# Kernel optimization log

Measured on AMD Instinct MI355X. Metric: run time of the kernel, lower is better.

Reference implementation:

```python
import jax, jax.numpy as jnp
import numpy as np

NUM_ENVS = 16384
N = 12          # decision vars (4 legs x 3D force)
M_CON = 24      # 4 SOC cones (3 each) + 12-dim hardtanh box
A_MIN, A_MAX = -10.0, 10.0
ALPHA, BETA = 1.0, 1.0


def setup_inputs() -> dict:
    key = jax.random.key(0)
    k1, k2, k3, k4 = jax.random.split(key, 4)
    Mw = jax.random.normal(k1, (NUM_ENVS, N, N), dtype=jnp.float32) / np.sqrt(N)
    # P must be SPD for inv/solve as in the original QP setup
    P = Mw @ jnp.swapaxes(Mw, -1, -2) + jnp.eye(N, dtype=jnp.float32)
    q = jax.random.normal(k2, (NUM_ENVS, N), dtype=jnp.float32)
    H = jax.random.normal(k3, (NUM_ENVS, M_CON, N), dtype=jnp.float32) * 0.5
    b = jax.random.normal(k4, (NUM_ENVS, M_CON), dtype=jnp.float32)
    contact_filter = jnp.ones((NUM_ENVS, M_CON), dtype=jnp.float32)
    return {"P": P, "q": q, "H": H, "b": b, "contact_filter": contact_filter, "iters": 100}


def _project(z, cf):
    # z: [B, m, 1]. Faithful to torch: project_onto_soc's only in-place effect on z
    # is z_part *= (z_part[:, 2:3] > 0); the full cone projection result is
    # discarded (returned but never written back). Then hardtanh box, then contact filter.
    Bsz = z.shape[0]
    soc = z[:, :12].reshape(Bsz, 4, 3)               # 4 cones of dim 3
    soc = soc * (soc[:, :, 2:3] > 0)                 # zero cone block if z-component <= 0
    box = jnp.clip(z[:, 12:24], A_MIN, A_MAX)        # hardtanh
    z = jnp.concatenate([soc.reshape(Bsz, 12, 1), box], axis=1)
    return z * cf


def reference(P, q, H, b, contact_filter, iters):
    m = H.shape[1]
    q_ = q[..., None]                                # [B, n, 1]
    b_ = b[..., None]                                # [B, m, 1]
    cf = contact_filter[..., None]                   # [B, m, 1]
    Ht = jnp.swapaxes(H, -1, -2)
    I = jnp.eye(m, dtype=P.dtype)
    Fm = I - H @ jnp.linalg.inv(P + Ht @ H) @ Ht     # [B, m, m]
    mu = Fm @ (H @ jnp.linalg.solve(P, q_) - b_)     # [B, m, 1]
    A = jnp.concatenate([
        jnp.concatenate([Fm, BETA * Fm], axis=2),
        jnp.concatenate([ALPHA * (I - 2.0 * Fm), I - 2.0 * ALPHA * BETA * Fm], axis=2),
    ], axis=1)                                       # [B, 2m, 2m]
    Bv = jnp.concatenate([BETA * mu, -2.0 * ALPHA * BETA * mu], axis=1)  # [B, 2m, 1]

    def step(lz, _):
        lz = A @ lz + Bv
        lz = jnp.concatenate([lz[:, :m], _project(lz[:, m:], cf)], axis=1)
        return lz, None

    lz0 = jnp.zeros((P.shape[0], 2 * m, 1), dtype=P.dtype)
    lz, _ = jax.lax.scan(step, lz0, None, length=iters)
    x = jnp.linalg.pinv(H) @ (lz[:, m:] - b_)        # [B, n, 1]
    return x, lz
```

## Files before the change

kernel.cpp:

```cpp
#include <hip/hip_runtime.h>

#define EPB 8
#define BLOCK 64
#define HS 292
#define GS 148
#define SS 28

#define WFENCE() __builtin_amdgcn_wave_barrier()

#define FMA4(acc, f, s)                                         \
  acc = fmaf((f).x, (s).x,                                      \
        fmaf((f).y, (s).y,                                      \
        fmaf((f).z, (s).z,                                      \
        fmaf((f).w, (s).w, (acc)))))

#define VFMA(acc, s, v)                                         \
  { (acc).x = fmaf((s), (v).x, (acc).x);                        \
    (acc).y = fmaf((s), (v).y, (acc).y);                        \
    (acc).z = fmaf((s), (v).z, (acc).z);                        \
    (acc).w = fmaf((s), (v).w, (acc).w); }

struct Row6 { float4 c0, c1, c2, c3, c4, c5; };

template<int K>
__device__ __forceinline__ float getel(const float4& a, const float4& b, const float4& c) {
  if constexpr (K == 0) return a.x; else if constexpr (K == 1) return a.y;
  else if constexpr (K == 2) return a.z; else if constexpr (K == 3) return a.w;
  else if constexpr (K == 4) return b.x; else if constexpr (K == 5) return b.y;
  else if constexpr (K == 6) return b.z; else if constexpr (K == 7) return b.w;
  else if constexpr (K == 8) return c.x; else if constexpr (K == 9) return c.y;
  else if constexpr (K == 10) return c.z; else return c.w;
}
template<int K>
__device__ __forceinline__ void setel(float4& a, float4& b, float4& c, float v) {
  if constexpr (K == 0) a.x = v; else if constexpr (K == 1) a.y = v;
  else if constexpr (K == 2) a.z = v; else if constexpr (K == 3) a.w = v;
  else if constexpr (K == 4) b.x = v; else if constexpr (K == 5) b.y = v;
  else if constexpr (K == 6) b.z = v; else if constexpr (K == 7) b.w = v;
  else if constexpr (K == 8) c.x = v; else if constexpr (K == 9) c.y = v;
  else if constexpr (K == 10) c.z = v; else c.w = v;
}

template<int K>
__device__ __forceinline__ void gj_step(float* A, int t) {
  if (t == K || t + 8 == K) {
    float4* r = (float4*)(A + K * 12);
    float4 a = r[0], b = r[1], c = r[2];
    float ip = 1.0f / getel<K>(a, b, c);
    setel<K>(a, b, c, 1.0f);
    a.x *= ip; a.y *= ip; a.z *= ip; a.w *= ip;
    b.x *= ip; b.y *= ip; b.z *= ip; b.w *= ip;
    c.x *= ip; c.y *= ip; c.z *= ip; c.w *= ip;
    r[0] = a; r[1] = b; r[2] = c;
  }
  WFENCE();
  const float4* pr = (const float4*)(A + K * 12);
  float4 p0 = pr[0], p1 = pr[1], p2 = pr[2];
  {
    float4* rr = (float4*)(A + t * 12);
    float4 a = rr[0], b = rr[1], c = rr[2];
    float f = getel<K>(a, b, c);
    if (t == K) f = 0.0f; else setel<K>(a, b, c, 0.0f);
    a.x = fmaf(-f, p0.x, a.x); a.y = fmaf(-f, p0.y, a.y);
    a.z = fmaf(-f, p0.z, a.z); a.w = fmaf(-f, p0.w, a.w);
    b.x = fmaf(-f, p1.x, b.x); b.y = fmaf(-f, p1.y, b.y);
    b.z = fmaf(-f, p1.z, b.z); b.w = fmaf(-f, p1.w, b.w);
    c.x = fmaf(-f, p2.x, c.x); c.y = fmaf(-f, p2.y, c.y);
    c.z = fmaf(-f, p2.z, c.z); c.w = fmaf(-f, p2.w, c.w);
    rr[0] = a; rr[1] = b; rr[2] = c;
  }
  if (t < 4) {
    const int i = t + 8;
    float4* rr = (float4*)(A + i * 12);
    float4 a = rr[0], b = rr[1], c = rr[2];
    float f = getel<K>(a, b, c);
    if (i == K) f = 0.0f; else setel<K>(a, b, c, 0.0f);
    a.x = fmaf(-f, p0.x, a.x); a.y = fmaf(-f, p0.y, a.y);
    a.z = fmaf(-f, p0.z, a.z); a.w = fmaf(-f, p0.w, a.w);
    b.x = fmaf(-f, p1.x, b.x); b.y = fmaf(-f, p1.y, b.y);
    b.z = fmaf(-f, p1.z, b.z); b.w = fmaf(-f, p1.w, b.w);
    c.x = fmaf(-f, p2.x, c.x); c.y = fmaf(-f, p2.y, c.y);
    c.z = fmaf(-f, p2.z, c.z); c.w = fmaf(-f, p2.w, c.w);
    rr[0] = a; rr[1] = b; rr[2] = c;
  }
  WFENCE();
}
template<int K>
__device__ __forceinline__ void gj_all(float* A, int t) {
  gj_step<K>(A, t);
  if constexpr (K < 11) gj_all<K + 1>(A, t);
}

__device__ __forceinline__ float dot12(float4 a0, float4 a1, float4 a2,
                                       const float* p) {
  const float4* p4 = (const float4*)p;
  float4 b0 = p4[0], b1 = p4[1], b2 = p4[2];
  float acc = 0.f;
  FMA4(acc, a0, b0); FMA4(acc, a1, b1); FMA4(acc, a2, b2);
  return acc;
}

__device__ __forceinline__ void build_gram_row(const float* myH, float* gi,
                                               int i, bool addP) {
  float4 a0 = {0,0,0,0}, a1 = {0,0,0,0}, a2 = {0,0,0,0};
#pragma unroll
  for (int k = 0; k < 24; ++k) {
    float coef = myH[k * 12 + i];
    const float4* hk = (const float4*)(myH + k * 12);
    float4 h0 = hk[0], h1 = hk[1], h2 = hk[2];
    VFMA(a0, coef, h0); VFMA(a1, coef, h1); VFMA(a2, coef, h2);
  }
  float4* g = (float4*)(gi + i * 12);
  if (addP) {
    float4 q0 = g[0], q1 = g[1], q2 = g[2];
    a0.x += q0.x; a0.y += q0.y; a0.z += q0.z; a0.w += q0.w;
    a1.x += q1.x; a1.y += q1.y; a1.z += q1.z; a1.w += q1.w;
    a2.x += q2.x; a2.y += q2.y; a2.z += q2.z; a2.w += q2.w;
  }
  g[0] = a0; g[1] = a1; g[2] = a2;
}

__device__ __forceinline__ Row6 build_row(const float* myH, const float* gi, int r) {
  const float4* hr4 = (const float4*)(myH + r * 12);
  float4 h0 = hr4[0], h1 = hr4[1], h2 = hr4[2];
  float4 gA = {0,0,0,0}, gB = {0,0,0,0}, gC = {0,0,0,0};
#define ACC_G(c, coef)                                          \
  { const float4* g4 = (const float4*)(gi + (c) * 12);          \
    float4 r0 = g4[0], r1 = g4[1], r2 = g4[2];                  \
    VFMA(gA, coef, r0); VFMA(gB, coef, r1); VFMA(gC, coef, r2); }
  ACC_G(0, h0.x) ACC_G(1, h0.y) ACC_G(2,  h0.z) ACC_G(3,  h0.w)
  ACC_G(4, h1.x) ACC_G(5, h1.y) ACC_G(6,  h1.z) ACC_G(7,  h1.w)
  ACC_G(8, h2.x) ACC_G(9, h2.y) ACC_G(10, h2.z) ACC_G(11, h2.w)
#undef ACC_G
  Row6 R;
#define FEL(j) ((((j) == r) ? 1.0f : 0.0f) - dot12(gA, gB, gC, myH + (j) * 12))
  R.c0 = make_float4(FEL(0),  FEL(1),  FEL(2),  FEL(3));
  R.c1 = make_float4(FEL(4),  FEL(5),  FEL(6),  FEL(7));
  R.c2 = make_float4(FEL(8),  FEL(9),  FEL(10), FEL(11));
  R.c3 = make_float4(FEL(12), FEL(13), FEL(14), FEL(15));
  R.c4 = make_float4(FEL(16), FEL(17), FEL(18), FEL(19));
  R.c5 = make_float4(FEL(20), FEL(21), FEL(22), FEL(23));
#undef FEL
  return R;
}

__global__ __launch_bounds__(BLOCK)
void pdhg_kernel(const float* __restrict__ P, const float* __restrict__ q,
                 const float* __restrict__ H, const float* __restrict__ b,
                 const float* __restrict__ cf, const int* __restrict__ itp,
                 float* __restrict__ out, int Btot) {
  __shared__ __align__(16) float sH[EPB * HS];
  __shared__ __align__(16) float sGi[EPB * GS];
  __shared__ __align__(16) float sS[EPB * SS];
  __shared__ __align__(16) float sAux[EPB * SS];

  const int tid = threadIdx.x;
  const int e   = tid >> 3;
  const int t   = tid & 7;
  const int env = blockIdx.x * EPB + e;
  const int niter = itp[0];
  const int r0w = 3 * t;

  {
    const float4* gH = (const float4*)(H + (size_t)blockIdx.x * EPB * 288);
#pragma unroll
    for (int rep = 0; rep < 9; ++rep) {
      int i = tid + rep * 64;
      int ee = i / 72, off = i - ee * 72;
      *(float4*)&sH[ee * HS + off * 4] = gH[i];
    }
    const float4* gP = (const float4*)(P + (size_t)blockIdx.x * EPB * 144);
#pragma unroll
    for (int rep = 0; rep < 4; ++rep) {
      int i = tid + rep * 64;
      int ee = i / 36, off = i - ee * 36;
      *(float4*)&sGi[ee * GS + off * 4] = gP[i];
    }
    { int i = tid + 256; if (tid < 32) {
        int ee = i / 36, off = i - ee * 36;
        *(float4*)&sGi[ee * GS + off * 4] = gP[i]; } }
    const float4* gq = (const float4*)(q + (size_t)blockIdx.x * EPB * 12);
    if (tid < EPB * 3) {
      int ee = tid / 3, off = tid - ee * 3;
      *(float4*)&sAux[ee * SS + off * 4] = gq[tid];
    }
    const float4* gb = (const float4*)(b + (size_t)blockIdx.x * EPB * 24);
    if (tid < EPB * 6) {
      int ee = tid / 6, off = tid - ee * 6;
      *(float4*)&sS[ee * SS + off * 4] = gb[tid];
    }
  }
  WFENCE();

  const float* myH = &sH[e * HS];
  float* giB = &sGi[e * GS];
  float* auxB = &sAux[e * SS];
  const float* bB = &sS[e * SS];

  build_gram_row(myH, giB, t, true);
  if (t < 4) build_gram_row(myH, giB, t + 8, true);
  WFENCE();
  gj_all<0>(giB, t);

  {
    const float4* gr = (const float4*)(giB + t * 12);
    auxB[12 + t] = dot12(gr[0], gr[1], gr[2], auxB);
    if (t < 4) {
      const float4* gr8 = (const float4*)(giB + (t + 8) * 12);
      auxB[12 + t + 8] = dot12(gr8[0], gr8[1], gr8[2], auxB);
    }
  }
  WFENCE();

  Row6 F0 = build_row(myH, giB, r0w + 0);
  Row6 F1 = build_row(myH, giB, r0w + 1);
  Row6 F2 = build_row(myH, giB, r0w + 2);
  float mu0, mu1, mu2;
  {
    const float4* h0 = (const float4*)(myH + (r0w + 0) * 12);
    const float4* h1 = (const float4*)(myH + (r0w + 1) * 12);
    const float4* h2 = (const float4*)(myH + (r0w + 2) * 12);
    const float* y = auxB + 12;
    float u0 = dot12(h0[0], h0[1], h0[2], y);
    float u1 = dot12(h1[0], h1[1], h1[2], y);
    float u2 = dot12(h2[0], h2[1], h2[2], y);
    const float4* bv = (const float4*)bB;
    float d0 = 0.f, d1 = 0.f, d2 = 0.f;
    float4 v;
    v = bv[0]; FMA4(d0, F0.c0, v); FMA4(d1, F1.c0, v); FMA4(d2, F2.c0, v);
    v = bv[1]; FMA4(d0, F0.c1, v); FMA4(d1, F1.c1, v); FMA4(d2, F2.c1, v);
    v = bv[2]; FMA4(d0, F0.c2, v); FMA4(d1, F1.c2, v); FMA4(d2, F2.c2, v);
    v = bv[3]; FMA4(d0, F0.c3, v); FMA4(d1, F1.c3, v); FMA4(d2, F2.c3, v);
    v = bv[4]; FMA4(d0, F0.c4, v); FMA4(d1, F1.c4, v); FMA4(d2, F2.c4, v);
    v = bv[5]; FMA4(d0, F0.c5, v); FMA4(d1, F1.c5, v); FMA4(d2, F2.c5, v);
    mu0 = u0 - d0;
    mu1 = u1 - d1;
    mu2 = u2 - d2;
  }
  float cfr0 = cf[(size_t)env * 24 + r0w];
  float cfr1 = cf[(size_t)env * 24 + r0w + 1];
  float cfr2 = cf[(size_t)env * 24 + r0w + 2];

  float l0 = 0.f, l1 = 0.f, l2 = 0.f, z0 = 0.f, z1 = 0.f, z2 = 0.f;
  float* sw = &sS[e * SS];
  for (int it = 0; it < niter; ++it) {
    float s0 = l0 + z0, s1 = l1 + z1, s2 = l2 + z2;
    sw[r0w] = s0; sw[r0w + 1] = s1; sw[r0w + 2] = s2;
    WFENCE();
    const float4* sv = (const float4*)sw;
    float w0 = mu0, w1 = mu1, w2 = mu2;
    float4 c;
    c = sv[0]; FMA4(w0, F0.c0, c); FMA4(w1, F1.c0, c); FMA4(w2, F2.c0, c);
    c = sv[1]; FMA4(w0, F0.c1, c); FMA4(w1, F1.c1, c); FMA4(w2, F2.c1, c);
    c = sv[2]; FMA4(w0, F0.c2, c); FMA4(w1, F1.c2, c); FMA4(w2, F2.c2, c);
    c = sv[3]; FMA4(w0, F0.c3, c); FMA4(w1, F1.c3, c); FMA4(w2, F2.c3, c);
    c = sv[4]; FMA4(w0, F0.c4, c); FMA4(w1, F1.c4, c); FMA4(w2, F2.c4, c);
    c = sv[5]; FMA4(w0, F0.c5, c); FMA4(w1, F1.c5, c); FMA4(w2, F2.c5, c);
    WFENCE();
    float zp0 = fmaf(-2.0f, w0, s0);
    float zp1 = fmaf(-2.0f, w1, s1);
    float zp2 = fmaf(-2.0f, w2, s2);
    l0 = w0; l1 = w1; l2 = w2;
    if (t < 4) {
      float m = (zp2 > 0.0f) ? 1.0f : 0.0f;
      z0 = zp0 * m * cfr0; z1 = zp1 * m * cfr1; z2 = zp2 * m * cfr2;
    } else {
      z0 = fminf(fmaxf(zp0, -10.0f), 10.0f) * cfr0;
      z1 = fminf(fmaxf(zp1, -10.0f), 10.0f) * cfr1;
      z2 = fminf(fmaxf(zp2, -10.0f), 10.0f) * cfr2;
    }
  }

  float* xout  = out;
  float* lzout = out + (size_t)Btot * 12;
  lzout[(size_t)env * 48 + r0w]          = l0;
  lzout[(size_t)env * 48 + r0w + 1]      = l1;
  lzout[(size_t)env * 48 + r0w + 2]      = l2;
  lzout[(size_t)env * 48 + 24 + r0w]     = z0;
  lzout[(size_t)env * 48 + 24 + r0w + 1] = z1;
  lzout[(size_t)env * 48 + 24 + r0w + 2] = z2;

  float bo0 = b[(size_t)env * 24 + r0w];
  float bo1 = b[(size_t)env * 24 + r0w + 1];
  float bo2 = b[(size_t)env * 24 + r0w + 2];
  WFENCE();
  auxB[r0w]     = z0 - bo0;
  auxB[r0w + 1] = z1 - bo1;
  auxB[r0w + 2] = z2 - bo2;
  WFENCE();

  float rv0 = 0.f, rv8 = 0.f;
#pragma unroll
  for (int k = 0; k < 24; ++k) rv0 = fmaf(myH[k * 12 + t], auxB[k], rv0);
  if (t < 4) {
#pragma unroll
    for (int k = 0; k < 24; ++k) rv8 = fmaf(myH[k * 12 + t + 8], auxB[k], rv8);
  }
  build_gram_row(myH, giB, t, false);
  if (t < 4) build_gram_row(myH, giB, t + 8, false);
  WFENCE();
  auxB[t] = rv0;
  if (t < 4) auxB[t + 8] = rv8;
  WFENCE();

  gj_all<0>(giB, t);
  {
    const float4* gr = (const float4*)(giB + t * 12);
    xout[(size_t)env * 12 + t] = dot12(gr[0], gr[1], gr[2], auxB);
    if (t < 4) {
      const float4* gr8 = (const float4*)(giB + (t + 8) * 12);
      xout[(size_t)env * 12 + t + 8] = dot12(gr8[0], gr8[1], gr8[2], auxB);
    }
  }
}

extern "C" void kernel_launch(void* const* d_in, const int* in_sizes, int n_in,
                              void* d_out, int out_size, void* d_ws, size_t ws_size,
                              hipStream_t stream) {
  const float* P  = (const float*)d_in[0];
  const float* q  = (const float*)d_in[1];
  const float* H  = (const float*)d_in[2];
  const float* b  = (const float*)d_in[3];
  const float* cf = (const float*)d_in[4];
  const int*   it = (const int*)d_in[5];
  float* out = (float*)d_out;
  const int B = in_sizes[1] / 12;
  const int grid = B / EPB;
  pdhg_kernel<<<grid, BLOCK, 0, stream>>>(P, q, H, b, cf, it, out, B);
}
```

Measured before the change: 156.7 us.

## Replace LDS vector exchange with DPP butterfly reduction in PDHG iteration

Each iteration used to write its three lane values of s to shared memory and read back all 24 before doing the row-times-vector products. The new loop relies on the symmetry of Fm. Each lane forms partial products for all 24 outputs from its own three s values, sums them across the 8 lanes of an environment with three DPP steps (xor1, xor2, half-mirror), then selects its three outputs with a tree of lane-bit conditionals. This removes the LDS round trip and the wave barriers from the serial iteration chain, at the cost of about 72 extra DPP adds per iteration and more register pressure.

```diff
diff --git a/kernel.cpp b/kernel.cpp
--- a/kernel.cpp
+++ b/kernel.cpp
@@ -8,6 +8,10 @@
 
 #define WFENCE() __builtin_amdgcn_wave_barrier()
 
+#define DPP_XOR1 0xB1
+#define DPP_XOR2 0x4E
+#define DPP_HMIR 0x141
+
 #define FMA4(acc, f, s)                                         \
   acc = fmaf((f).x, (s).x,                                      \
         fmaf((f).y, (s).y,                                      \
@@ -20,7 +24,22 @@
     (acc).z = fmaf((s), (v).z, (acc).z);                        \
     (acc).w = fmaf((s), (v).w, (acc).w); }
 
-struct Row6 { float4 c0, c1, c2, c3, c4, c5; };
+struct Row6  { float4 a, b, c, d, e, f; };
+struct Vec24 { float4 a, b, c, d, e, f; };
+
+template<int CTRL>
+__device__ __forceinline__ float dppv(float v) {
+  return __int_as_float(__builtin_amdgcn_update_dpp(
+      0, __float_as_int(v), CTRL, 0xF, 0xF, true));
+}
+
+#define APPLY24(OP)                                              \
+  OP(a, x) OP(a, y) OP(a, z) OP(a, w)                            \
+  OP(b, x) OP(b, y) OP(b, z) OP(b, w)                            \
+  OP(c, x) OP(c, y) OP(c, z) OP(c, w)                            \
+  OP(d, x) OP(d, y) OP(d, z) OP(d, w)                            \
+  OP(e, x) OP(e, y) OP(e, z) OP(e, w)                            \
+  OP(f, x) OP(f, y) OP(f, z) OP(f, w)
 
 template<int K>
 __device__ __forceinline__ float getel(const float4& a, const float4& b, const float4& c) {
@@ -134,12 +153,12 @@
 #undef ACC_G
   Row6 R;
 #define FEL(j) ((((j) == r) ? 1.0f : 0.0f) - dot12(gA, gB, gC, myH + (j) * 12))
-  R.c0 = make_float4(FEL(0),  FEL(1),  FEL(2),  FEL(3));
-  R.c1 = make_float4(FEL(4),  FEL(5),  FEL(6),  FEL(7));
-  R.c2 = make_float4(FEL(8),  FEL(9),  FEL(10), FEL(11));
-  R.c3 = make_float4(FEL(12), FEL(13), FEL(14), FEL(15));
-  R.c4 = make_float4(FEL(16), FEL(17), FEL(18), FEL(19));
-  R.c5 = make_float4(FEL(20), FEL(21), FEL(22), FEL(23));
+  R.a = make_float4(FEL(0),  FEL(1),  FEL(2),  FEL(3));
+  R.b = make_float4(FEL(4),  FEL(5),  FEL(6),  FEL(7));
+  R.c = make_float4(FEL(8),  FEL(9),  FEL(10), FEL(11));
+  R.d = make_float4(FEL(12), FEL(13), FEL(14), FEL(15));
+  R.e = make_float4(FEL(16), FEL(17), FEL(18), FEL(19));
+  R.f = make_float4(FEL(20), FEL(21), FEL(22), FEL(23));
 #undef FEL
   return R;
 }
@@ -151,7 +170,7 @@
                  float* __restrict__ out, int Btot) {
   __shared__ __align__(16) float sH[EPB * HS];
   __shared__ __align__(16) float sGi[EPB * GS];
-  __shared__ __align__(16) float sS[EPB * SS];
+  __shared__ __align__(16) float sB[EPB * SS];
   __shared__ __align__(16) float sAux[EPB * SS];
 
   const int tid = threadIdx.x;
@@ -187,7 +206,7 @@
     const float4* gb = (const float4*)(b + (size_t)blockIdx.x * EPB * 24);
     if (tid < EPB * 6) {
       int ee = tid / 6, off = tid - ee * 6;
-      *(float4*)&sS[ee * SS + off * 4] = gb[tid];
+      *(float4*)&sB[ee * SS + off * 4] = gb[tid];
     }
   }
   WFENCE();
@@ -195,7 +214,7 @@
   const float* myH = &sH[e * HS];
   float* giB = &sGi[e * GS];
   float* auxB = &sAux[e * SS];
-  const float* bB = &sS[e * SS];
+  const float* bB = &sB[e * SS];
 
   build_gram_row(myH, giB, t, true);
   if (t < 4) build_gram_row(myH, giB, t + 8, true);
@@ -212,9 +231,9 @@
   }
   WFENCE();
 
-  Row6 F0 = build_row(myH, giB, r0w + 0);
-  Row6 F1 = build_row(myH, giB, r0w + 1);
-  Row6 F2 = build_row(myH, giB, r0w + 2);
+  Row6 Fc0 = build_row(myH, giB, r0w + 0);
+  Row6 Fc1 = build_row(myH, giB, r0w + 1);
+  Row6 Fc2 = build_row(myH, giB, r0w + 2);
   float mu0, mu1, mu2;
   {
     const float4* h0 = (const float4*)(myH + (r0w + 0) * 12);
@@ -227,12 +246,12 @@
     const float4* bv = (const float4*)bB;
     float d0 = 0.f, d1 = 0.f, d2 = 0.f;
     float4 v;
-    v = bv[0]; FMA4(d0, F0.c0, v); FMA4(d1, F1.c0, v); FMA4(d2, F2.c0, v);
-    v = bv[1]; FMA4(d0, F0.c1, v); FMA4(d1, F1.c1, v); FMA4(d2, F2.c1, v);
-    v = bv[2]; FMA4(d0, F0.c2, v); FMA4(d1, F1.c2, v); FMA4(d2, F2.c2, v);
-    v = bv[3]; FMA4(d0, F0.c3, v); FMA4(d1, F1.c3, v); FMA4(d2, F2.c3, v);
-    v = bv[4]; FMA4(d0, F0.c4, v); FMA4(d1, F1.c4, v); FMA4(d2, F2.c4, v);
-    v = bv[5]; FMA4(d0, F0.c5, v); FMA4(d1, F1.c5, v); FMA4(d2, F2.c5, v);
+    v = bv[0]; FMA4(d0, Fc0.a, v); FMA4(d1, Fc1.a, v); FMA4(d2, Fc2.a, v);
+    v = bv[1]; FMA4(d0, Fc0.b, v); FMA4(d1, Fc1.b, v); FMA4(d2, Fc2.b, v);
+    v = bv[2]; FMA4(d0, Fc0.c, v); FMA4(d1, Fc1.c, v); FMA4(d2, Fc2.c, v);
+    v = bv[3]; FMA4(d0, Fc0.d, v); FMA4(d1, Fc1.d, v); FMA4(d2, Fc2.d, v);
+    v = bv[4]; FMA4(d0, Fc0.e, v); FMA4(d1, Fc1.e, v); FMA4(d2, Fc2.e, v);
+    v = bv[5]; FMA4(d0, Fc0.f, v); FMA4(d1, Fc1.f, v); FMA4(d2, Fc2.f, v);
     mu0 = u0 - d0;
     mu1 = u1 - d1;
     mu2 = u2 - d2;
@@ -241,22 +260,42 @@
   float cfr1 = cf[(size_t)env * 24 + r0w + 1];
   float cfr2 = cf[(size_t)env * 24 + r0w + 2];
 
+  const bool tb0 = (t & 1) != 0;
+  const bool tb1 = (t & 2) != 0;
+  const bool tb2 = (t & 4) != 0;
+
   float l0 = 0.f, l1 = 0.f, l2 = 0.f, z0 = 0.f, z1 = 0.f, z2 = 0.f;
-  float* sw = &sS[e * SS];
   for (int it = 0; it < niter; ++it) {
     float s0 = l0 + z0, s1 = l1 + z1, s2 = l2 + z2;
-    sw[r0w] = s0; sw[r0w + 1] = s1; sw[r0w + 2] = s2;
-    WFENCE();
-    const float4* sv = (const float4*)sw;
-    float w0 = mu0, w1 = mu1, w2 = mu2;
-    float4 c;
-    c = sv[0]; FMA4(w0, F0.c0, c); FMA4(w1, F1.c0, c); FMA4(w2, F2.c0, c);
-    c = sv[1]; FMA4(w0, F0.c1, c); FMA4(w1, F1.c1, c); FMA4(w2, F2.c1, c);
-    c = sv[2]; FMA4(w0, F0.c2, c); FMA4(w1, F1.c2, c); FMA4(w2, F2.c2, c);
-    c = sv[3]; FMA4(w0, F0.c3, c); FMA4(w1, F1.c3, c); FMA4(w2, F2.c3, c);
-    c = sv[4]; FMA4(w0, F0.c4, c); FMA4(w1, F1.c4, c); FMA4(w2, F2.c4, c);
-    c = sv[5]; FMA4(w0, F0.c5, c); FMA4(w1, F1.c5, c); FMA4(w2, F2.c5, c);
-    WFENCE();
+    Vec24 Y;
+#define YFMA(C, X) Y.C.X = fmaf(Fc2.C.X, s2, fmaf(Fc1.C.X, s1, Fc0.C.X * s0));
+    APPLY24(YFMA)
+#undef YFMA
+#define YR1(C, X) Y.C.X += dppv<DPP_XOR1>(Y.C.X);
+    APPLY24(YR1)
+#undef YR1
+#define YR2(C, X) Y.C.X += dppv<DPP_XOR2>(Y.C.X);
+    APPLY24(YR2)
+#undef YR2
+#define YR3(C, X) Y.C.X += dppv<DPP_HMIR>(Y.C.X);
+    APPLY24(YR3)
+#undef YR3
+    float w0, w1, w2;
+    {
+      float a_, b_, c_, d_, e_, f_;
+      a_ = tb0 ? Y.a.w : Y.a.x;  b_ = tb0 ? Y.c.y : Y.b.z;
+      c_ = tb0 ? Y.d.w : Y.d.x;  d_ = tb0 ? Y.f.y : Y.e.z;
+      e_ = tb1 ? b_ : a_;        f_ = tb1 ? d_ : c_;
+      w0 = (tb2 ? f_ : e_) + mu0;
+      a_ = tb0 ? Y.b.x : Y.a.y;  b_ = tb0 ? Y.c.z : Y.b.w;
+      c_ = tb0 ? Y.e.x : Y.d.y;  d_ = tb0 ? Y.f.z : Y.e.w;
+      e_ = tb1 ? b_ : a_;        f_ = tb1 ? d_ : c_;
+      w1 = (tb2 ? f_ : e_) + mu1;
+      a_ = tb0 ? Y.b.y : Y.a.z;  b_ = tb0 ? Y.c.w : Y.c.x;
+      c_ = tb0 ? Y.e.y : Y.d.z;  d_ = tb0 ? Y.f.w : Y.f.x;
+      e_ = tb1 ? b_ : a_;        f_ = tb1 ? d_ : c_;
+      w2 = (tb2 ? f_ : e_) + mu2;
+    }
     float zp0 = fmaf(-2.0f, w0, s0);
     float zp1 = fmaf(-2.0f, w1, s1);
     float zp2 = fmaf(-2.0f, w2, s2);
```

After: 193.3 us. +23.3%, slower.
